# Kernel tuning notes

Hardware: AMD Instinct MI355X
Metric: run time of the kernel (lower is better)

Reference implementation:

```python
import jax, jax.numpy as jnp
import numpy as np

B, N, NONGT, D, H, PE = 128, 36, 36, 1024, 16, 64
DG = D // H  # per-head dim = 64


def setup_inputs() -> dict:
    key = jax.random.key(0)
    ks = jax.random.split(key, 10)
    s = 0.02
    return {
        "roi_feat": jax.random.normal(ks[0], (B, N, D), jnp.float32),
        "adj_matrix": jax.random.randint(ks[1], (B, N, NONGT), 0, 2, jnp.int32),
        "position_embedding": jax.random.normal(ks[2], (B, N, NONGT, PE), jnp.float32),
        "label_biases_att": jax.random.normal(ks[3], (B, N, NONGT), jnp.float32) * 0.1,
        # effective (weight-normed) linear weights
        "Wq": jax.random.normal(ks[4], (D, D), jnp.float32) * s,
        "bq": jnp.zeros((D,), jnp.float32),
        "Wk": jax.random.normal(ks[5], (D, D), jnp.float32) * s,
        "bk": jnp.zeros((D,), jnp.float32),
        "Wpos": jax.random.normal(ks[6], (H, PE), jnp.float32) * s,
        "bpos": jnp.zeros((H,), jnp.float32),
        # grouped 1x1 conv (groups=H): per-head projection feat_dim -> feat_dim/H
        "Wout": jax.random.normal(ks[7], (H, DG, D), jnp.float32) * s,
        "bout": jnp.zeros((D,), jnp.float32),
    }


def reference(roi_feat, adj_matrix, position_embedding, label_biases_att,
              Wq, bq, Wk, bk, Wpos, bpos, Wout, bout):
    b, n, d = roi_feat.shape
    nongt = adj_matrix.shape[2]
    dg = d // H
    v = roi_feat[:, :nongt, :]                                  # [B,nongt,D]
    q = (roi_feat @ Wq.T + bq).reshape(b, n, H, dg)             # [B,N,H,dg]
    k = (v @ Wk.T + bk).reshape(b, nongt, H, dg)                # [B,nongt,H,dg]
    # scaled QK^T, laid out [B,N,H,nongt] (orig: matmul then transpose(1,2))
    aff = jnp.einsum('bnhd,bmhd->bnhm', q, k) / jnp.sqrt(jnp.float32(dg))
    # position log-bias
    pos = jax.nn.relu(position_embedding.reshape(b, n * nongt, -1) @ Wpos.T + bpos)
    pos = pos.reshape(b, n, nongt, H).transpose(0, 1, 3, 2)     # [B,N,H,nongt]
    waff = aff + jnp.log(jnp.maximum(pos, jnp.float32(1e-6)))
    # adjacency mask + label bias (orig does this in [B,N,nongt,H] layout; equivalent)
    mask = adj_matrix[:, :, None, :] > 0                        # [B,N,1,nongt]
    waff = jnp.where(mask, waff, jnp.float32(-9e15)) + label_biases_att[:, :, None, :]
    att = jax.nn.softmax(waff, axis=-1)                         # [B,N,H,nongt]
    # weighted sum of full V (note: V is full feat_dim per head, not dg)
    out_t = jnp.einsum('bnhm,bmd->bnhd', att, v)                # [B,N,H,D]
    # grouped 1x1 conv: per-head D -> D/H, heads concatenated
    out = jnp.einsum('bnhd,hed->bnhe', out_t, Wout).reshape(b, n, d) + bout
    return out
```

## Files before the change

kernel.cpp:

```cpp
#include <hip/hip_runtime.h>
#include <hip/hip_bf16.h>

#define BB 128
#define NN 36
#define DD 1024
#define HH 16
#define ROWS (BB*NN)
#define NCOLS (3*DD)

typedef __attribute__((ext_vector_type(8))) __bf16 bf16x8;
typedef __attribute__((ext_vector_type(4))) float f32x4;
typedef __attribute__((ext_vector_type(4))) unsigned short us4;
typedef __attribute__((ext_vector_type(8))) unsigned short us8;

__device__ inline unsigned short f2bf(float f) {
    __hip_bfloat16 h = __float2bfloat16(f);
    return *reinterpret_cast<unsigned short*>(&h);
}

__device__ inline void async16(const unsigned short* g, unsigned short* l) {
    __builtin_amdgcn_global_load_lds((const __attribute__((address_space(1))) unsigned int*)g,
                                     (__attribute__((address_space(3))) unsigned int*)l, 16, 0, 0);
}

__global__ __launch_bounds__(256) void prep_kernel(const float* __restrict__ roi,
                                                   const float* __restrict__ Wq,
                                                   const float* __restrict__ Wk,
                                                   const float* __restrict__ Wout,
                                                   const float* __restrict__ pe,
                                                   const float* __restrict__ Wpos,
                                                   const float* __restrict__ bpos,
                                                   const int* __restrict__ adj,
                                                   const float* __restrict__ lbl,
                                                   unsigned short* __restrict__ roi_bf,
                                                   unsigned short* __restrict__ Wcat_bf,
                                                   float* __restrict__ extra) {
    const int bid = blockIdx.x, tid = threadIdx.x;
    if (bid < 4608) {
        int i = bid * 256 + tid;
        f32x4 v = ((const f32x4*)roi)[i];
        us4 o;
        o.x = f2bf(v[0]); o.y = f2bf(v[1]); o.z = f2bf(v[2]); o.w = f2bf(v[3]);
        ((us4*)roi_bf)[i] = o;
        return;
    }
    if (bid < 7680) {
        int wb = bid - 4608;
        int sel = wb >> 10;
        const float* src = sel == 0 ? Wq : (sel == 1 ? Wk : Wout);
        int i = (wb & 1023) * 256 + tid;
        f32x4 v = ((const f32x4*)src)[i];
        us4 o;
        o.x = f2bf(v[0]); o.y = f2bf(v[1]); o.z = f2bf(v[2]); o.w = f2bf(v[3]);
        ((us4*)(Wcat_bf + (size_t)sel * DD * DD))[i] = o;
        return;
    }
    __shared__ __align__(16) float wps[HH * 64];
    __shared__ float bps[HH];
    for (int i = tid; i < HH * 64; i += 256) wps[i] = Wpos[i];
    if (tid < HH) bps[tid] = bpos[tid];
    __syncthreads();

    int idx = (bid - 7680) * 256 + tid;
    f32x4 pr[16];
    const f32x4* pv = (const f32x4*)(pe + (size_t)idx * 64);
#pragma unroll
    for (int j = 0; j < 16; j++) pr[j] = pv[j];
    int a = adj[idx];
    float add = lbl[idx] + (a > 0 ? 0.f : -9e15f);
    int b = idx / 1296, nm = idx % 1296;
    size_t obase = (size_t)b * (16 * 1296) + nm;
    for (int hh = 0; hh < 16; hh++) {
        const f32x4* wv = (const f32x4*)(wps + hh * 64);
        f32x4 acc4 = {0.f, 0.f, 0.f, 0.f};
#pragma unroll
        for (int j = 0; j < 16; j++) acc4 += pr[j] * wv[j];
        float d = acc4[0] + acc4[1] + acc4[2] + acc4[3] + bps[hh];
        d = fmaxf(d, 0.f);
        d = __logf(fmaxf(d, 1e-6f));
        extra[obase + (size_t)hh * 1296] = d + add;
    }
}

__global__ __launch_bounds__(256) void gemm_kernel(const unsigned short* __restrict__ A,
                                                   const unsigned short* __restrict__ Bm,
                                                   const float* __restrict__ bq,
                                                   const float* __restrict__ bk,
                                                   unsigned short* __restrict__ P) {
    __shared__ __align__(16) unsigned short smem[12288];
    unsigned short* As = smem;
    unsigned short* Bs = smem + 8192;
    unsigned short* Cs = smem;

    const int tid  = threadIdx.x;
    const int n0   = (blockIdx.x % 48) * 64;
    const int m0   = (blockIdx.x / 48) * 128;
    const int wave = tid >> 6, lane = tid & 63;
    const int quad = lane >> 4, l16 = lane & 15;
    const int wm = (wave & 1) * 64, wn = (wave >> 1) * 32;

    int arow[4], acol[4], brow[2], bcol[2];
#pragma unroll
    for (int p = 0; p < 4; p++) {
        int c = wave * 256 + p * 64 + lane;
        arow[p] = c >> 3;
        acol[p] = ((c & 7) ^ (arow[p] & 7)) * 8;
    }
#pragma unroll
    for (int p = 0; p < 2; p++) {
        int c = wave * 128 + p * 64 + lane;
        brow[p] = c >> 3;
        bcol[p] = ((c & 7) ^ (brow[p] & 7)) * 8;
    }

    f32x4 acc[4][2] = {};

    for (int k0 = 0; k0 < DD; k0 += 64) {
#pragma unroll
        for (int p = 0; p < 4; p++)
            async16(A + (size_t)(m0 + arow[p]) * DD + k0 + acol[p], As + wave * 2048 + p * 512);
#pragma unroll
        for (int p = 0; p < 2; p++)
            async16(Bm + (size_t)(n0 + brow[p]) * DD + k0 + bcol[p], Bs + wave * 1024 + p * 512);
        __syncthreads();

#pragma unroll
        for (int ks = 0; ks < 2; ks++) {
            int kch = ks * 4 + quad;
            bf16x8 af[4], bf[2];
#pragma unroll
            for (int mi = 0; mi < 4; mi++) {
                int row = wm + mi * 16 + l16;
                af[mi] = *(const bf16x8*)&As[row * 64 + ((kch ^ (row & 7)) * 8)];
            }
#pragma unroll
            for (int ni = 0; ni < 2; ni++) {
                int row = wn + ni * 16 + l16;
                bf[ni] = *(const bf16x8*)&Bs[row * 64 + ((kch ^ (row & 7)) * 8)];
            }
#pragma unroll
            for (int mi = 0; mi < 4; mi++)
#pragma unroll
                for (int ni = 0; ni < 2; ni++)
                    acc[mi][ni] = __builtin_amdgcn_mfma_f32_16x16x32_bf16(af[mi], bf[ni], acc[mi][ni], 0, 0, 0);
        }
        __syncthreads();
    }

    float bias[2];
#pragma unroll
    for (int ni = 0; ni < 2; ni++) {
        int colg = n0 + wn + ni * 16 + l16;
        bias[ni] = (colg < DD) ? bq[colg] : ((colg < 2 * DD) ? bk[colg - DD] : 0.f);
    }
#pragma unroll
    for (int mi = 0; mi < 4; mi++)
#pragma unroll
        for (int ni = 0; ni < 2; ni++) {
            int row = wm + mi * 16 + quad * 4;
            int col = wn + ni * 16 + l16;
#pragma unroll
            for (int r = 0; r < 4; r++)
                Cs[(row + r) * 72 + col] = f2bf(acc[mi][ni][r] + bias[ni]);
        }
    __syncthreads();
#pragma unroll
    for (int i = 0; i < 4; i++) {
        int ch = i * 256 + tid;
        int row = ch >> 3, cc = (ch & 7) * 8;
        us8 v = *(const us8*)&Cs[row * 72 + cc];
        *(us8*)&P[(size_t)(m0 + row) * NCOLS + n0 + cc] = v;
    }
}

#define VS 72
__global__ __launch_bounds__(64) void attn_kernel(const unsigned short* __restrict__ P,
                                                  const float* __restrict__ extra,
                                                  const float* __restrict__ bout,
                                                  float* __restrict__ out) {
    const int b = blockIdx.x >> 4;
    const int h = blockIdx.x & 15;
    __shared__ __align__(16) unsigned short smem_att[(64 + 48) * VS];
    __shared__ __align__(16) float exs[1296];
    unsigned short* vwT  = smem_att;
    unsigned short* atts = smem_att + 64 * VS;
    float* osT = (float*)smem_att;
    const int lane = threadIdx.x;
    const int quad = lane >> 4, l16 = lane & 15;
    const size_t pbase = (size_t)b * NN * NCOLS;

    us4 vreg[9];
#pragma unroll
    for (int i = 0; i < 9; i++) {
        int idx = i * 64 + lane;
        int m = idx >> 4, e0 = (idx & 15) * 4;
        vreg[i] = *(const us4*)&P[pbase + (size_t)m * NCOLS + 2 * DD + h * 64 + e0];
    }
    const f32x4* exg = (const f32x4*)(extra + (size_t)blockIdx.x * 1296);
    f32x4 ereg[6];
#pragma unroll
    for (int i = 0; i < 6; i++) {
        int idx = i * 64 + lane;
        if (idx < 324) ereg[i] = exg[idx];
    }

    const unsigned short* Pq = P + pbase + h * 64;
    const unsigned short* Pk = Pq + DD;
    int rq[3];
#pragma unroll
    for (int t = 0; t < 3; t++) { int rr = t * 16 + l16; rq[t] = rr < 36 ? rr : 35; }

    f32x4 aff[3][3] = {};
#pragma unroll
    for (int ks = 0; ks < 64; ks += 32) {
        bf16x8 afr[3], bfr[3];
#pragma unroll
        for (int t = 0; t < 3; t++) afr[t] = *(const bf16x8*)&Pq[(size_t)rq[t] * NCOLS + ks + quad * 8];
#pragma unroll
        for (int t = 0; t < 3; t++) bfr[t] = *(const bf16x8*)&Pk[(size_t)rq[t] * NCOLS + ks + quad * 8];
#pragma unroll
        for (int mt = 0; mt < 3; mt++)
#pragma unroll
            for (int nt = 0; nt < 3; nt++)
                aff[mt][nt] = __builtin_amdgcn_mfma_f32_16x16x32_bf16(afr[mt], bfr[nt], aff[mt][nt], 0, 0, 0);
    }

    for (int i = lane; i < 64 * 28; i += 64) vwT[(i / 28) * VS + 36 + (i % 28)] = 0;
    for (int i = lane; i < 48 * 16; i += 64) atts[(i >> 4) * VS + 48 + (i & 15)] = 0;
#pragma unroll
    for (int i = 0; i < 9; i++) {
        int idx = i * 64 + lane;
        int m = idx >> 4, e0 = (idx & 15) * 4;
        vwT[(e0 + 0) * VS + m] = vreg[i].x;
        vwT[(e0 + 1) * VS + m] = vreg[i].y;
        vwT[(e0 + 2) * VS + m] = vreg[i].z;
        vwT[(e0 + 3) * VS + m] = vreg[i].w;
    }
#pragma unroll
    for (int i = 0; i < 6; i++) {
        int idx = i * 64 + lane;
        if (idx < 324) ((f32x4*)exs)[idx] = ereg[i];
    }
    __syncthreads();

#pragma unroll
    for (int mt = 0; mt < 3; mt++) {
#pragma unroll
        for (int r = 0; r < 4; r++) {
            int row = mt * 16 + quad * 4 + r;
            float w[3];
#pragma unroll
            for (int nt = 0; nt < 3; nt++) {
                int col = nt * 16 + l16;
                bool valid = (row < 36) && (col < 36);
                w[nt] = valid ? (aff[mt][nt][r] * 0.125f + exs[row * 36 + col]) : -3.4e38f;
            }
            float mx = fmaxf(fmaxf(w[0], w[1]), w[2]);
#pragma unroll
            for (int d = 1; d < 16; d <<= 1) mx = fmaxf(mx, __shfl_xor(mx, d));
            float e0 = __expf(w[0] - mx), e1 = __expf(w[1] - mx), e2 = __expf(w[2] - mx);
            float s = e0 + e1 + e2;
#pragma unroll
            for (int d = 1; d < 16; d <<= 1) s += __shfl_xor(s, d);
            float rs = 1.0f / s;
            atts[row * VS + 0  + l16] = f2bf(e0 * rs);
            atts[row * VS + 16 + l16] = f2bf(e1 * rs);
            atts[row * VS + 32 + l16] = f2bf(e2 * rs);
        }
    }
    __syncthreads();

    f32x4 o[3][4] = {};
#pragma unroll
    for (int ks = 0; ks < 64; ks += 32) {
        bf16x8 pa[3], pb[4];
#pragma unroll
        for (int mt = 0; mt < 3; mt++) pa[mt] = *(const bf16x8*)&atts[(mt * 16 + l16) * VS + ks + quad * 8];
#pragma unroll
        for (int nt = 0; nt < 4; nt++) pb[nt] = *(const bf16x8*)&vwT[(nt * 16 + l16) * VS + ks + quad * 8];
#pragma unroll
        for (int mt = 0; mt < 3; mt++)
#pragma unroll
            for (int nt = 0; nt < 4; nt++)
                o[mt][nt] = __builtin_amdgcn_mfma_f32_16x16x32_bf16(pa[mt], pb[nt], o[mt][nt], 0, 0, 0);
    }
    __syncthreads();

    float bo[4];
#pragma unroll
    for (int nt = 0; nt < 4; nt++) bo[nt] = bout[h * 64 + nt * 16 + l16];
#pragma unroll
    for (int mt = 0; mt < 3; mt++)
#pragma unroll
        for (int r = 0; r < 4; r++) {
            int n = mt * 16 + quad * 4 + r;
            if (n < 36) {
#pragma unroll
                for (int nt = 0; nt < 4; nt++)
                    osT[n * 68 + nt * 16 + l16] = o[mt][nt][r] + bo[nt];
            }
        }
    __syncthreads();
#pragma unroll
    for (int i = 0; i < 9; i++) {
        int ch = i * 64 + lane;
        int n = ch >> 4, c = (ch & 15) * 4;
        f32x4 v = *(const f32x4*)&osT[n * 68 + c];
        *(f32x4*)&out[(size_t)(b * NN + n) * DD + h * 64 + c] = v;
    }
}

extern "C" void kernel_launch(void* const* d_in, const int* in_sizes, int n_in,
                              void* d_out, int out_size, void* d_ws, size_t ws_size,
                              hipStream_t stream) {
    const float* roi  = (const float*)d_in[0];
    const int*   adj  = (const int*)  d_in[1];
    const float* pe   = (const float*)d_in[2];
    const float* lbl  = (const float*)d_in[3];
    const float* Wq   = (const float*)d_in[4];
    const float* bq   = (const float*)d_in[5];
    const float* Wk   = (const float*)d_in[6];
    const float* bk   = (const float*)d_in[7];
    const float* Wpos = (const float*)d_in[8];
    const float* bpos = (const float*)d_in[9];
    const float* Wout = (const float*)d_in[10];
    const float* bout = (const float*)d_in[11];
    float* out = (float*)d_out;

    char* w = (char*)d_ws;
    unsigned short* roi_bf  = (unsigned short*)(w);
    unsigned short* Wcat_bf = (unsigned short*)(w + 9437184);
    unsigned short* P       = (unsigned short*)(w + 15728640);
    float*          extra   = (float*)(w + 44040192);

    prep_kernel<<<8328, 256, 0, stream>>>(roi, Wq, Wk, Wout, pe, Wpos, bpos, adj, lbl,
                                          roi_bf, Wcat_bf, extra);
    gemm_kernel<<<36 * 48, 256, 0, stream>>>(roi_bf, Wcat_bf, bq, bk, P);
    attn_kernel<<<BB * HH, 64, 0, stream>>>(P, extra, bout, out);
}
```

Baseline: 203.7 us.

## Fuse QKV projection GEMM with per-head attention in one kernel

Replaces the separate QKV GEMM and attention kernels with a single kernel. Each block computes the Q, K and V projections for 4 batches (144 rows) and one head, keeping them in LDS, then runs softmax attention per wave. This removes the round trip of the projection matrix P through global memory and one kernel launch. In exchange there are only 512 blocks with large register and LDS footprints, which lowers occupancy, and the roi tile is reloaded for each of the 16 heads.

Result: faster. 177.9 us (-12.7%).

```diff
diff --git a/kernel.cpp b/kernel.cpp
--- a/kernel.cpp
+++ b/kernel.cpp
@@ -6,12 +6,10 @@
 #define DD 1024
 #define HH 16
 #define ROWS (BB*NN)
-#define NCOLS (3*DD)
 
 typedef __attribute__((ext_vector_type(8))) __bf16 bf16x8;
 typedef __attribute__((ext_vector_type(4))) float f32x4;
 typedef __attribute__((ext_vector_type(4))) unsigned short us4;
-typedef __attribute__((ext_vector_type(8))) unsigned short us8;
 
 __device__ inline unsigned short f2bf(float f) {
     __hip_bfloat16 h = __float2bfloat16(f);
@@ -82,142 +80,104 @@
     }
 }
 
-__global__ __launch_bounds__(256) void gemm_kernel(const unsigned short* __restrict__ A,
-                                                   const unsigned short* __restrict__ Bm,
-                                                   const float* __restrict__ bq,
-                                                   const float* __restrict__ bk,
-                                                   unsigned short* __restrict__ P) {
-    __shared__ __align__(16) unsigned short smem[12288];
-    unsigned short* As = smem;
-    unsigned short* Bs = smem + 8192;
-    unsigned short* Cs = smem;
-
+__global__ __launch_bounds__(256, 2) void fused_kernel(const unsigned short* __restrict__ A,
+                                                       const unsigned short* __restrict__ Wc,
+                                                       const float* __restrict__ bq,
+                                                       const float* __restrict__ bk,
+                                                       const float* __restrict__ extra,
+                                                       const float* __restrict__ bout,
+                                                       float* __restrict__ out) {
+    __shared__ __align__(16) unsigned short pool[32256];
     const int tid  = threadIdx.x;
-    const int n0   = (blockIdx.x % 48) * 64;
-    const int m0   = (blockIdx.x / 48) * 128;
     const int wave = tid >> 6, lane = tid & 63;
     const int quad = lane >> 4, l16 = lane & 15;
-    const int wm = (wave & 1) * 64, wn = (wave >> 1) * 32;
-
-    int arow[4], acol[4], brow[2], bcol[2];
-#pragma unroll
-    for (int p = 0; p < 4; p++) {
-        int c = wave * 256 + p * 64 + lane;
-        arow[p] = c >> 3;
-        acol[p] = ((c & 7) ^ (arow[p] & 7)) * 8;
-    }
-#pragma unroll
-    for (int p = 0; p < 2; p++) {
-        int c = wave * 128 + p * 64 + lane;
-        brow[p] = c >> 3;
-        bcol[p] = ((c & 7) ^ (brow[p] & 7)) * 8;
-    }
-
-    f32x4 acc[4][2] = {};
+    const int h  = blockIdx.x & 15;
+    const int bg = blockIdx.x >> 4;
+    const int row0 = bg * 144;
+
+    unsigned short* As = pool;
+    unsigned short* Bs = pool + 9216;
+
+    f32x4 acc[9][3] = {};
+    const int cnt = (wave < 2) ? 11 : 10;
 
     for (int k0 = 0; k0 < DD; k0 += 64) {
-#pragma unroll
-        for (int p = 0; p < 4; p++)
-            async16(A + (size_t)(m0 + arow[p]) * DD + k0 + acol[p], As + wave * 2048 + p * 512);
-#pragma unroll
-        for (int p = 0; p < 2; p++)
-            async16(Bm + (size_t)(n0 + brow[p]) * DD + k0 + bcol[p], Bs + wave * 1024 + p * 512);
+        for (int i = 0; i < cnt; i++) {
+            int j = wave + 4 * i;
+            int c = j * 64 + lane;
+            if (j < 18) {
+                int row = c >> 3;
+                int col = ((c & 7) ^ (row & 7)) * 8;
+                async16(A + (size_t)(row0 + row) * DD + k0 + col, As + j * 512);
+            } else {
+                int cb = c - 1152;
+                int row = cb >> 3;
+                int sec = row >> 6;
+                int wrow = sec * DD + h * 64 + (row & 63);
+                int col = ((cb & 7) ^ (row & 7)) * 8;
+                async16(Wc + (size_t)wrow * DD + k0 + col, Bs + (j - 18) * 512);
+            }
+        }
         __syncthreads();
 
 #pragma unroll
         for (int ks = 0; ks < 2; ks++) {
             int kch = ks * 4 + quad;
-            bf16x8 af[4], bf[2];
-#pragma unroll
-            for (int mi = 0; mi < 4; mi++) {
-                int row = wm + mi * 16 + l16;
-                af[mi] = *(const bf16x8*)&As[row * 64 + ((kch ^ (row & 7)) * 8)];
-            }
-#pragma unroll
-            for (int ni = 0; ni < 2; ni++) {
-                int row = wn + ni * 16 + l16;
-                bf[ni] = *(const bf16x8*)&Bs[row * 64 + ((kch ^ (row & 7)) * 8)];
-            }
-#pragma unroll
-            for (int mi = 0; mi < 4; mi++)
-#pragma unroll
-                for (int ni = 0; ni < 2; ni++)
-                    acc[mi][ni] = __builtin_amdgcn_mfma_f32_16x16x32_bf16(af[mi], bf[ni], acc[mi][ni], 0, 0, 0);
+            bf16x8 bfv[3], afv[9];
+#pragma unroll
+            for (int ct = 0; ct < 3; ct++) {
+                int rowb = wave * 48 + ct * 16 + l16;
+                bfv[ct] = *(const bf16x8*)&Bs[rowb * 64 + ((kch ^ (rowb & 7)) * 8)];
+            }
+#pragma unroll
+            for (int rt = 0; rt < 9; rt++) {
+                int rowa = rt * 16 + l16;
+                afv[rt] = *(const bf16x8*)&As[rowa * 64 + ((kch ^ (rowa & 7)) * 8)];
+            }
+#pragma unroll
+            for (int rt = 0; rt < 9; rt++)
+#pragma unroll
+                for (int ct = 0; ct < 3; ct++)
+                    acc[rt][ct] = __builtin_amdgcn_mfma_f32_16x16x32_bf16(afv[rt], bfv[ct], acc[rt][ct], 0, 0, 0);
         }
         __syncthreads();
     }
 
-    float bias[2];
-#pragma unroll
-    for (int ni = 0; ni < 2; ni++) {
-        int colg = n0 + wn + ni * 16 + l16;
-        bias[ni] = (colg < DD) ? bq[colg] : ((colg < 2 * DD) ? bk[colg - DD] : 0.f);
-    }
-#pragma unroll
-    for (int mi = 0; mi < 4; mi++)
-#pragma unroll
-        for (int ni = 0; ni < 2; ni++) {
-            int row = wm + mi * 16 + quad * 4;
-            int col = wn + ni * 16 + l16;
-#pragma unroll
-            for (int r = 0; r < 4; r++)
-                Cs[(row + r) * 72 + col] = f2bf(acc[mi][ni][r] + bias[ni]);
-        }
+    unsigned short* qL = pool;
+    unsigned short* kL = pool + 10368;
+#pragma unroll
+    for (int ct = 0; ct < 3; ct++) {
+        int g = wave * 48 + ct * 16 + l16;
+        int sec = g >> 6, e = g & 63;
+        if (sec < 2) {
+            unsigned short* dst = (sec == 0) ? qL : kL;
+            float bias = (sec == 0) ? bq[h * 64 + e] : bk[h * 64 + e];
+#pragma unroll
+            for (int rt = 0; rt < 9; rt++)
+#pragma unroll
+                for (int r = 0; r < 4; r++) {
+                    int row = rt * 16 + quad * 4 + r;
+                    dst[row * 72 + e] = f2bf(acc[rt][ct][r] + bias);
+                }
+        }
+    }
     __syncthreads();
-#pragma unroll
-    for (int i = 0; i < 4; i++) {
-        int ch = i * 256 + tid;
-        int row = ch >> 3, cc = (ch & 7) * 8;
-        us8 v = *(const us8*)&Cs[row * 72 + cc];
-        *(us8*)&P[(size_t)(m0 + row) * NCOLS + n0 + cc] = v;
-    }
-}
-
-#define VS 72
-__global__ __launch_bounds__(64) void attn_kernel(const unsigned short* __restrict__ P,
-                                                  const float* __restrict__ extra,
-                                                  const float* __restrict__ bout,
-                                                  float* __restrict__ out) {
-    const int b = blockIdx.x >> 4;
-    const int h = blockIdx.x & 15;
-    __shared__ __align__(16) unsigned short smem_att[(64 + 48) * VS];
-    __shared__ __align__(16) float exs[1296];
-    unsigned short* vwT  = smem_att;
-    unsigned short* atts = smem_att + 64 * VS;
-    float* osT = (float*)smem_att;
-    const int lane = threadIdx.x;
-    const int quad = lane >> 4, l16 = lane & 15;
-    const size_t pbase = (size_t)b * NN * NCOLS;
-
-    us4 vreg[9];
-#pragma unroll
-    for (int i = 0; i < 9; i++) {
-        int idx = i * 64 + lane;
-        int m = idx >> 4, e0 = (idx & 15) * 4;
-        vreg[i] = *(const us4*)&P[pbase + (size_t)m * NCOLS + 2 * DD + h * 64 + e0];
-    }
-    const f32x4* exg = (const f32x4*)(extra + (size_t)blockIdx.x * 1296);
-    f32x4 ereg[6];
-#pragma unroll
-    for (int i = 0; i < 6; i++) {
-        int idx = i * 64 + lane;
-        if (idx < 324) ereg[i] = exg[idx];
-    }
-
-    const unsigned short* Pq = P + pbase + h * 64;
-    const unsigned short* Pk = Pq + DD;
+
+    const int bat = wave;
+    const unsigned short* qB = qL + bat * 36 * 72;
+    const unsigned short* kB = kL + bat * 36 * 72;
     int rq[3];
 #pragma unroll
     for (int t = 0; t < 3; t++) { int rr = t * 16 + l16; rq[t] = rr < 36 ? rr : 35; }
 
     f32x4 aff[3][3] = {};
 #pragma unroll
-    for (int ks = 0; ks < 64; ks += 32) {
+    for (int ks = 0; ks < 2; ks++) {
         bf16x8 afr[3], bfr[3];
 #pragma unroll
-        for (int t = 0; t < 3; t++) afr[t] = *(const bf16x8*)&Pq[(size_t)rq[t] * NCOLS + ks + quad * 8];
-#pragma unroll
-        for (int t = 0; t < 3; t++) bfr[t] = *(const bf16x8*)&Pk[(size_t)rq[t] * NCOLS + ks + quad * 8];
+        for (int t = 0; t < 3; t++) afr[t] = *(const bf16x8*)&qB[rq[t] * 72 + ks * 32 + quad * 8];
+#pragma unroll
+        for (int t = 0; t < 3; t++) bfr[t] = *(const bf16x8*)&kB[rq[t] * 72 + ks * 32 + quad * 8];
 #pragma unroll
         for (int mt = 0; mt < 3; mt++)
 #pragma unroll
@@ -225,24 +185,23 @@
                 aff[mt][nt] = __builtin_amdgcn_mfma_f32_16x16x32_bf16(afr[mt], bfr[nt], aff[mt][nt], 0, 0, 0);
     }
 
-    for (int i = lane; i < 64 * 28; i += 64) vwT[(i / 28) * VS + 36 + (i % 28)] = 0;
-    for (int i = lane; i < 48 * 16; i += 64) atts[(i >> 4) * VS + 48 + (i & 15)] = 0;
-#pragma unroll
-    for (int i = 0; i < 9; i++) {
-        int idx = i * 64 + lane;
-        int m = idx >> 4, e0 = (idx & 15) * 4;
-        vwT[(e0 + 0) * VS + m] = vreg[i].x;
-        vwT[(e0 + 1) * VS + m] = vreg[i].y;
-        vwT[(e0 + 2) * VS + m] = vreg[i].z;
-        vwT[(e0 + 3) * VS + m] = vreg[i].w;
-    }
-#pragma unroll
-    for (int i = 0; i < 6; i++) {
-        int idx = i * 64 + lane;
-        if (idx < 324) ((f32x4*)exs)[idx] = ereg[i];
-    }
+    const float* exb = extra + ((size_t)((bg * 4 + bat) * 16 + h)) * 1296;
+    float exv[3][4][3];
+#pragma unroll
+    for (int mt = 0; mt < 3; mt++)
+#pragma unroll
+        for (int r = 0; r < 4; r++) {
+            int row = mt * 16 + quad * 4 + r;
+#pragma unroll
+            for (int nt = 0; nt < 3; nt++) {
+                int col = nt * 16 + l16;
+                exv[mt][r][nt] = (row < 36 && col < 36) ? exb[row * 36 + col] : 0.f;
+            }
+        }
     __syncthreads();
 
+    unsigned short* vwT   = pool;
+    unsigned short* attsL = pool + 18432 + bat * 3456;
 #pragma unroll
     for (int mt = 0; mt < 3; mt++) {
 #pragma unroll
@@ -253,7 +212,7 @@
             for (int nt = 0; nt < 3; nt++) {
                 int col = nt * 16 + l16;
                 bool valid = (row < 36) && (col < 36);
-                w[nt] = valid ? (aff[mt][nt][r] * 0.125f + exs[row * 36 + col]) : -3.4e38f;
+                w[nt] = valid ? (aff[mt][nt][r] * 0.125f + exv[mt][r][nt]) : -3.4e38f;
             }
             float mx = fmaxf(fmaxf(w[0], w[1]), w[2]);
 #pragma unroll
@@ -263,32 +222,53 @@
 #pragma unroll
             for (int d = 1; d < 16; d <<= 1) s += __shfl_xor(s, d);
             float rs = 1.0f / s;
-            atts[row * VS + 0  + l16] = f2bf(e0 * rs);
-            atts[row * VS + 16 + l16] = f2bf(e1 * rs);
-            atts[row * VS + 32 + l16] = f2bf(e2 * rs);
-        }
+            attsL[row * 72 + 0  + l16] = f2bf(e0 * rs);
+            attsL[row * 72 + 16 + l16] = f2bf(e1 * rs);
+            attsL[row * 72 + 32 + l16] = f2bf(e2 * rs);
+        }
+    }
+    for (int i = lane; i < 48 * 16; i += 64) attsL[(i >> 4) * 72 + 48 + (i & 15)] = 0;
+#pragma unroll
+    for (int ct = 0; ct < 3; ct++) {
+        int g = wave * 48 + ct * 16 + l16;
+        int sec = g >> 6, e = g & 63;
+        if (sec == 2) {
+#pragma unroll
+            for (int rt = 0; rt < 9; rt++)
+#pragma unroll
+                for (int r = 0; r < 4; r++) {
+                    int row = rt * 16 + quad * 4 + r;
+                    int bb = row / 36, m = row - bb * 36;
+                    vwT[bb * 4608 + e * 72 + m] = f2bf(acc[rt][ct][r]);
+                }
+        }
+    }
+    {
+        unsigned short* vB = vwT + bat * 4608;
+        for (int m = 36; m < 64; m++) vB[lane * 72 + m] = 0;
     }
     __syncthreads();
 
+    const unsigned short* vB = vwT + bat * 4608;
     f32x4 o[3][4] = {};
 #pragma unroll
-    for (int ks = 0; ks < 64; ks += 32) {
+    for (int ks = 0; ks < 2; ks++) {
         bf16x8 pa[3], pb[4];
 #pragma unroll
-        for (int mt = 0; mt < 3; mt++) pa[mt] = *(const bf16x8*)&atts[(mt * 16 + l16) * VS + ks + quad * 8];
-#pragma unroll
-        for (int nt = 0; nt < 4; nt++) pb[nt] = *(const bf16x8*)&vwT[(nt * 16 + l16) * VS + ks + quad * 8];
+        for (int mt = 0; mt < 3; mt++) pa[mt] = *(const bf16x8*)&attsL[(mt * 16 + l16) * 72 + ks * 32 + quad * 8];
+#pragma unroll
+        for (int nt = 0; nt < 4; nt++) pb[nt] = *(const bf16x8*)&vB[(nt * 16 + l16) * 72 + ks * 32 + quad * 8];
 #pragma unroll
         for (int mt = 0; mt < 3; mt++)
 #pragma unroll
             for (int nt = 0; nt < 4; nt++)
                 o[mt][nt] = __builtin_amdgcn_mfma_f32_16x16x32_bf16(pa[mt], pb[nt], o[mt][nt], 0, 0, 0);
     }
-    __syncthreads();
 
     float bo[4];
 #pragma unroll
     for (int nt = 0; nt < 4; nt++) bo[nt] = bout[h * 64 + nt * 16 + l16];
+    const size_t obase = (size_t)((bg * 4 + bat) * 36) * DD + h * 64;
 #pragma unroll
     for (int mt = 0; mt < 3; mt++)
 #pragma unroll
@@ -297,17 +277,9 @@
             if (n < 36) {
 #pragma unroll
                 for (int nt = 0; nt < 4; nt++)
-                    osT[n * 68 + nt * 16 + l16] = o[mt][nt][r] + bo[nt];
-            }
-        }
-    __syncthreads();
-#pragma unroll
-    for (int i = 0; i < 9; i++) {
-        int ch = i * 64 + lane;
-        int n = ch >> 4, c = (ch & 15) * 4;
-        f32x4 v = *(const f32x4*)&osT[n * 68 + c];
-        *(f32x4*)&out[(size_t)(b * NN + n) * DD + h * 64 + c] = v;
-    }
+                    out[obase + (size_t)n * DD + nt * 16 + l16] = o[mt][nt][r] + bo[nt];
+            }
+        }
 }
 
 extern "C" void kernel_launch(void* const* d_in, const int* in_sizes, int n_in,
@@ -330,11 +302,9 @@
     char* w = (char*)d_ws;
     unsigned short* roi_bf  = (unsigned short*)(w);
     unsigned short* Wcat_bf = (unsigned short*)(w + 9437184);
-    unsigned short* P       = (unsigned short*)(w + 15728640);
-    float*          extra   = (float*)(w + 44040192);
+    float*          extra   = (float*)(w + 15728640);
 
     prep_kernel<<<8328, 256, 0, stream>>>(roi, Wq, Wk, Wout, pe, Wpos, bpos, adj, lbl,
                                           roi_bf, Wcat_bf, extra);
-    gemm_kernel<<<36 * 48, 256, 0, stream>>>(roi_bf, Wcat_bf, bq, bk, P);
-    attn_kernel<<<BB * HH, 64, 0, stream>>>(P, extra, bout, out);
-}
+    fused_kernel<<<32 * 16, 256, 0, stream>>>(roi_bf, Wcat_bf, bq, bk, extra, bout, out);
+}
```
